# Kernel optimization log

Measured on AMD Instinct MI355X. Metric: run time of the kernel, lower is better.

The kernel has to match this reference:

```python
import jax, jax.numpy as jnp
import numpy as np
from jax.ops import segment_sum

N_NODES = 50000
N_EDGES = 800000
IN_CH, HIDDEN, OUT_CH = 64, 128, 64


def _glorot(key, fan_in, fan_out):
    lim = np.sqrt(6.0 / (fan_in + fan_out)).astype(np.float32)
    return jax.random.uniform(key, (fan_in, fan_out), jnp.float32, -lim, lim)


def setup_inputs() -> dict:
    key = jax.random.key(0)
    ks = jax.random.split(key, 10)
    x = jax.random.normal(ks[0], (N_NODES, IN_CH), jnp.float32)
    edge_index = jax.random.randint(ks[1], (2, N_EDGES), 0, N_NODES, jnp.int64)
    return {
        "x": x,
        "edge_index": edge_index,
        # GINConv1 MLP: Linear(in,hidden) -> ReLU -> Linear(hidden,hidden)
        "W1": _glorot(ks[2], IN_CH, HIDDEN),
        "b1": jnp.zeros((HIDDEN,), jnp.float32),
        "W2": _glorot(ks[3], HIDDEN, HIDDEN),
        "b2": jnp.zeros((HIDDEN,), jnp.float32),
        "eps1": jnp.zeros((), jnp.float32),
        # GINConv2 MLP: Linear(hidden,hidden) -> ReLU -> Linear(hidden,out)
        "W3": _glorot(ks[4], HIDDEN, HIDDEN),
        "b3": jnp.zeros((HIDDEN,), jnp.float32),
        "W4": _glorot(ks[5], HIDDEN, OUT_CH),
        "b4": jnp.zeros((OUT_CH,), jnp.float32),
        "eps2": jnp.zeros((), jnp.float32),
    }


def _gin_conv(x, src, dst, eps, Wa, ba, Wb, bb):
    # message = x[src]; aggregate = scatter-add at dst (sum aggregation)
    agg = segment_sum(x[src], dst, num_segments=N_NODES)  # [N, C]
    h = (1.0 + eps) * x + agg
    h = jax.nn.relu(h @ Wa + ba)
    return h @ Wb + bb


def reference(x, edge_index, W1, b1, W2, b2, eps1, W3, b3, W4, b4, eps2):
    src, dst = edge_index[0], edge_index[1]
    h1 = jax.nn.relu(_gin_conv(x, src, dst, eps1, W1, b1, W2, b2))
    h2 = _gin_conv(h1, src, dst, eps2, W3, b3, W4, b4)
    return h2
```

## Files before the change

kernel.cpp:

```cpp
#include <hip/hip_runtime.h>

#define N_NODES 50000
#define N_EDGES 800000
#define IN_CH 64
#define HIDDEN 128
#define OUT_CH 64
#define CAP 64

typedef unsigned short ushort_t;
typedef unsigned int uint_t;
typedef __attribute__((ext_vector_type(8))) short short8;
typedef __attribute__((ext_vector_type(4))) float f32x4;

__device__ __forceinline__ float bits2f(unsigned int u16) {
    union { unsigned int i; float f; } v;
    v.i = (u16 & 0xFFFFu) << 16;
    return v.f;
}

__device__ __forceinline__ ushort_t f2bits(float f) {
    union { float f; unsigned int i; } v;
    v.f = f;
    unsigned int x = v.i;
    if ((x & 0x7F800000u) == 0x7F800000u) return (ushort_t)(x >> 16);
    unsigned int r = (x + 0x7FFFu + ((x >> 16) & 1u)) >> 16;
    return (ushort_t)r;
}

__device__ __forceinline__ uint_t pack2(float x, float y) {
    return (uint_t)f2bits(x) | ((uint_t)f2bits(y) << 16);
}

__global__ __launch_bounds__(256) void append_k(const int* __restrict__ ei,
                                                int* __restrict__ cnt,
                                                ushort_t* __restrict__ bucket) {
    int e = blockIdx.x * 256 + threadIdx.x;
    if (e >= N_EDGES) return;
    int src = ei[e];
    int dst = ei[N_EDGES + e];
    int pos = atomicAdd(&cnt[dst], 1);
    if (pos < CAP) bucket[(size_t)dst * CAP + pos] = (ushort_t)src;
}

__global__ __launch_bounds__(256) void cvt_k(const float* __restrict__ x,
                                             uint_t* __restrict__ xu) {
    int i = blockIdx.x * 256 + threadIdx.x;
    if (i >= N_NODES * IN_CH / 2) return;
    float2 v = ((const float2*)x)[i];
    xu[i] = pack2(v.x, v.y);
}

__global__ __launch_bounds__(256) void pack_k(const float* __restrict__ W,
                                              ushort_t* __restrict__ out,
                                              int K, int C) {
    int tid = blockIdx.x * 256 + threadIdx.x;
    if (tid >= K * C) return;
    int j = tid & 7;
    int l = (tid >> 3) & 63;
    int rest = tid >> 9;
    int KC = K >> 5;
    int kc = rest % KC;
    int nt = rest / KC;
    int k = kc * 32 + (l >> 4) * 8 + j;
    int n = nt * 16 + (l & 15);
    out[tid] = f2bits(W[(size_t)k * C + n]);
}

__global__ __launch_bounds__(256) void gather1(const uint_t* __restrict__ xu,
                                               const int* __restrict__ cnt,
                                               const ushort_t* __restrict__ bucket,
                                               const float* __restrict__ eps1,
                                               uint_t* __restrict__ agg1b) {
    int tid = threadIdx.x;
    int li = tid & 31;
    int n = blockIdx.x * 8 + (tid >> 5);
    uint_t v = xu[(size_t)n * 32 + li];
    float se = 1.0f + eps1[0];
    float a0 = se * bits2f(v), a1 = se * bits2f(v >> 16);
    float b0 = 0.f, b1 = 0.f, c0 = 0.f, c1 = 0.f, d0 = 0.f, d1 = 0.f;
    int cn = cnt[n]; if (cn > CAP) cn = CAP;
    const ushort_t* bk = bucket + (size_t)n * CAP;
    int i = 0;
    for (; i + 3 < cn; i += 4) {
        ushort4 e4 = *(const ushort4*)(bk + i);
        uint_t u0 = xu[(size_t)e4.x * 32 + li];
        uint_t u1 = xu[(size_t)e4.y * 32 + li];
        uint_t u2 = xu[(size_t)e4.z * 32 + li];
        uint_t u3 = xu[(size_t)e4.w * 32 + li];
        a0 += bits2f(u0); a1 += bits2f(u0 >> 16);
        b0 += bits2f(u1); b1 += bits2f(u1 >> 16);
        c0 += bits2f(u2); c1 += bits2f(u2 >> 16);
        d0 += bits2f(u3); d1 += bits2f(u3 >> 16);
    }
    for (; i < cn; i++) {
        uint_t u = xu[(size_t)bk[i] * 32 + li];
        a0 += bits2f(u); a1 += bits2f(u >> 16);
    }
    agg1b[(size_t)n * 32 + li] = pack2(a0 + b0 + c0 + d0, a1 + b1 + c1 + d1);
}

__global__ __launch_bounds__(256) void gather2(const ushort_t* __restrict__ h1,
                                               const int* __restrict__ cnt,
                                               const ushort_t* __restrict__ bucket,
                                               const float* __restrict__ eps2,
                                               uint_t* __restrict__ agg2b) {
    int lane = threadIdx.x & 63;
    int n = blockIdx.x * 4 + (threadIdx.x >> 6);
    const uint_t* h1u = (const uint_t*)h1;
    uint_t v = h1u[(size_t)n * 64 + lane];
    float se = 1.0f + eps2[0];
    float a0 = se * bits2f(v), a1 = se * bits2f(v >> 16);
    float b0 = 0.f, b1 = 0.f, c0 = 0.f, c1 = 0.f, d0 = 0.f, d1 = 0.f;
    int cn = cnt[n]; if (cn > CAP) cn = CAP;
    const ushort_t* bk = bucket + (size_t)n * CAP;
    int i = 0;
    for (; i + 3 < cn; i += 4) {
        ushort4 e4 = *(const ushort4*)(bk + i);
        uint_t u0 = h1u[(size_t)e4.x * 64 + lane];
        uint_t u1 = h1u[(size_t)e4.y * 64 + lane];
        uint_t u2 = h1u[(size_t)e4.z * 64 + lane];
        uint_t u3 = h1u[(size_t)e4.w * 64 + lane];
        a0 += bits2f(u0); a1 += bits2f(u0 >> 16);
        b0 += bits2f(u1); b1 += bits2f(u1 >> 16);
        c0 += bits2f(u2); c1 += bits2f(u2 >> 16);
        d0 += bits2f(u3); d1 += bits2f(u3 >> 16);
    }
    for (; i < cn; i++) {
        uint_t u = h1u[(size_t)bk[i] * 64 + lane];
        a0 += bits2f(u); a1 += bits2f(u >> 16);
    }
    agg2b[(size_t)n * 64 + lane] = pack2(a0 + b0 + c0 + d0, a1 + b1 + c1 + d1);
}

#define TPAD 136

__global__ __launch_bounds__(256) void mlp1(const ushort_t* __restrict__ agg1b,
                                            const ushort_t* __restrict__ pW1,
                                            const float* __restrict__ b1,
                                            const ushort_t* __restrict__ pW2,
                                            const float* __restrict__ b2,
                                            ushort_t* __restrict__ h1) {
    __shared__ __align__(16) ushort_t t[64][TPAD];
    int w = threadIdx.x >> 6;
    int l = threadIdx.x & 63;
    int q = l >> 4;
    int c = l & 15;
    int m0 = blockIdx.x * 64 + w * 16;
    int node = m0 + c;
    int nc = node < N_NODES ? node : 0;
    short8 a0 = *(const short8*)(agg1b + (size_t)nc * IN_CH + q * 8);
    short8 a1 = *(const short8*)(agg1b + (size_t)nc * IN_CH + 32 + q * 8);
#pragma unroll
    for (int nt = 0; nt < 8; nt++) {
        float bb = b1[nt * 16 + c];
        f32x4 acc = {bb, bb, bb, bb};
        short8 bf0 = *(const short8*)(pW1 + (size_t)((nt * 2 + 0) * 64 + l) * 8);
        short8 bf1 = *(const short8*)(pW1 + (size_t)((nt * 2 + 1) * 64 + l) * 8);
        acc = __builtin_amdgcn_mfma_f32_16x16x32_bf16(a0, bf0, acc, 0, 0, 0);
        acc = __builtin_amdgcn_mfma_f32_16x16x32_bf16(a1, bf1, acc, 0, 0, 0);
#pragma unroll
        for (int r = 0; r < 4; r++)
            t[w * 16 + q * 4 + r][nt * 16 + c] = f2bits(fmaxf(acc[r], 0.0f));
    }
    __syncthreads();
    short8 A[4];
#pragma unroll
    for (int kc = 0; kc < 4; kc++)
        A[kc] = *(const short8*)&t[w * 16 + c][kc * 32 + q * 8];
#pragma unroll
    for (int nt = 0; nt < 8; nt++) {
        float bb = b2[nt * 16 + c];
        f32x4 acc = {bb, bb, bb, bb};
#pragma unroll
        for (int kc = 0; kc < 4; kc++) {
            short8 bf = *(const short8*)(pW2 + (size_t)((nt * 4 + kc) * 64 + l) * 8);
            acc = __builtin_amdgcn_mfma_f32_16x16x32_bf16(A[kc], bf, acc, 0, 0, 0);
        }
#pragma unroll
        for (int r = 0; r < 4; r++) {
            int rr = m0 + q * 4 + r;
            if (rr < N_NODES)
                h1[(size_t)rr * HIDDEN + nt * 16 + c] = f2bits(fmaxf(acc[r], 0.0f));
        }
    }
}

__global__ __launch_bounds__(256) void mlp2(const ushort_t* __restrict__ agg2b,
                                            const ushort_t* __restrict__ pW3,
                                            const float* __restrict__ b3,
                                            const ushort_t* __restrict__ pW4,
                                            const float* __restrict__ b4,
                                            float* __restrict__ out) {
    __shared__ __align__(16) ushort_t t[64][TPAD];
    int w = threadIdx.x >> 6;
    int l = threadIdx.x & 63;
    int q = l >> 4;
    int c = l & 15;
    int m0 = blockIdx.x * 64 + w * 16;
    int node = m0 + c;
    int nc = node < N_NODES ? node : 0;
    short8 A[4];
#pragma unroll
    for (int kc = 0; kc < 4; kc++)
        A[kc] = *(const short8*)(agg2b + (size_t)nc * HIDDEN + kc * 32 + q * 8);
#pragma unroll
    for (int nt = 0; nt < 8; nt++) {
        float bb = b3[nt * 16 + c];
        f32x4 acc = {bb, bb, bb, bb};
#pragma unroll
        for (int kc = 0; kc < 4; kc++) {
            short8 bf = *(const short8*)(pW3 + (size_t)((nt * 4 + kc) * 64 + l) * 8);
            acc = __builtin_amdgcn_mfma_f32_16x16x32_bf16(A[kc], bf, acc, 0, 0, 0);
        }
#pragma unroll
        for (int r = 0; r < 4; r++)
            t[w * 16 + q * 4 + r][nt * 16 + c] = f2bits(fmaxf(acc[r], 0.0f));
    }
    __syncthreads();
    short8 B[4];
#pragma unroll
    for (int kc = 0; kc < 4; kc++)
        B[kc] = *(const short8*)&t[w * 16 + c][kc * 32 + q * 8];
#pragma unroll
    for (int nt = 0; nt < 4; nt++) {
        float bb = b4[nt * 16 + c];
        f32x4 acc = {bb, bb, bb, bb};
#pragma unroll
        for (int kc = 0; kc < 4; kc++) {
            short8 bf = *(const short8*)(pW4 + (size_t)((nt * 4 + kc) * 64 + l) * 8);
            acc = __builtin_amdgcn_mfma_f32_16x16x32_bf16(B[kc], bf, acc, 0, 0, 0);
        }
#pragma unroll
        for (int r = 0; r < 4; r++) {
            int rr = m0 + q * 4 + r;
            if (rr < N_NODES)
                out[(size_t)rr * OUT_CH + nt * 16 + c] = acc[r];
        }
    }
}

extern "C" void kernel_launch(void* const* d_in, const int* in_sizes, int n_in,
                              void* d_out, int out_size, void* d_ws, size_t ws_size,
                              hipStream_t stream) {
    const float* x    = (const float*)d_in[0];
    const int*   ei   = (const int*)d_in[1];
    const float* W1   = (const float*)d_in[2];
    const float* b1   = (const float*)d_in[3];
    const float* W2   = (const float*)d_in[4];
    const float* b2   = (const float*)d_in[5];
    const float* eps1 = (const float*)d_in[6];
    const float* W3   = (const float*)d_in[7];
    const float* b3   = (const float*)d_in[8];
    const float* W4   = (const float*)d_in[9];
    const float* b4   = (const float*)d_in[10];
    const float* eps2 = (const float*)d_in[11];
    float* out = (float*)d_out;

    ushort_t* wsU = (ushort_t*)d_ws;
    ushort_t* agg2b = wsU;
    uint_t*   xb    = (uint_t*)wsU;
    ushort_t* h1    = wsU + (size_t)6400000;
    ushort_t* agg1b = wsU + (size_t)12800000;
    ushort_t* pW    = wsU + (size_t)16000000;
    ushort_t* pW1 = pW;
    ushort_t* pW2 = pW + 8192;
    ushort_t* pW3 = pW + 24576;
    ushort_t* pW4 = pW + 40960;
    int* cnt        = (int*)(wsU + (size_t)16049152);
    ushort_t* bucket = (ushort_t*)(cnt + N_NODES);

    hipMemsetAsync(cnt, 0, N_NODES * sizeof(int), stream);
    append_k<<<(N_EDGES + 255) / 256, 256, 0, stream>>>(ei, cnt, bucket);

    pack_k<<<(IN_CH * HIDDEN + 255) / 256, 256, 0, stream>>>(W1, pW1, IN_CH, HIDDEN);
    pack_k<<<(HIDDEN * HIDDEN + 255) / 256, 256, 0, stream>>>(W2, pW2, HIDDEN, HIDDEN);
    pack_k<<<(HIDDEN * HIDDEN + 255) / 256, 256, 0, stream>>>(W3, pW3, HIDDEN, HIDDEN);
    pack_k<<<(HIDDEN * OUT_CH + 255) / 256, 256, 0, stream>>>(W4, pW4, HIDDEN, OUT_CH);

    cvt_k<<<(N_NODES * IN_CH / 2 + 255) / 256, 256, 0, stream>>>(x, xb);
    gather1<<<N_NODES / 8, 256, 0, stream>>>(xb, cnt, bucket, eps1, (uint_t*)agg1b);
    mlp1<<<(N_NODES + 63) / 64, 256, 0, stream>>>(agg1b, pW1, b1, pW2, b2, h1);

    gather2<<<N_NODES / 4, 256, 0, stream>>>(h1, cnt, bucket, eps2, (uint_t*)agg2b);
    mlp2<<<(N_NODES + 63) / 64, 256, 0, stream>>>(agg2b, pW3, b3, pW4, b4, out);
}
```

Before: 229.0 us.

## Build CSR buckets via two-pass LDS binning and fuse prep kernels

Replaces the global-atomic edge append with a two-stage binning scheme. First, blocks bin edges by destination range into shared memory and flush them to per-bin segments. Second, one block per 256-node bin builds the bucket list in LDS and writes it out with coalesced vector stores. The memset, weight-pack kernels and x conversion are merged into fewer launches. The goal is to cut scattered global atomics and launch overhead. The cost is an extra pass over the edges and a fixed per-bin segment capacity that could overflow.

After: 198.0 us. 1.16x faster.

```diff
diff --git a/kernel.cpp b/kernel.cpp
--- a/kernel.cpp
+++ b/kernel.cpp
@@ -6,6 +6,10 @@
 #define HIDDEN 128
 #define OUT_CH 64
 #define CAP 64
+#define BINS 196
+#define CHUNK 3125
+#define LCAP 48
+#define SEGCAP 4608
 
 typedef unsigned short ushort_t;
 typedef unsigned int uint_t;
@@ -31,39 +35,103 @@
     return (uint_t)f2bits(x) | ((uint_t)f2bits(y) << 16);
 }
 
-__global__ __launch_bounds__(256) void append_k(const int* __restrict__ ei,
-                                                int* __restrict__ cnt,
-                                                ushort_t* __restrict__ bucket) {
-    int e = blockIdx.x * 256 + threadIdx.x;
-    if (e >= N_EDGES) return;
-    int src = ei[e];
-    int dst = ei[N_EDGES + e];
-    int pos = atomicAdd(&cnt[dst], 1);
-    if (pos < CAP) bucket[(size_t)dst * CAP + pos] = (ushort_t)src;
-}
-
-__global__ __launch_bounds__(256) void cvt_k(const float* __restrict__ x,
-                                             uint_t* __restrict__ xu) {
-    int i = blockIdx.x * 256 + threadIdx.x;
-    if (i >= N_NODES * IN_CH / 2) return;
-    float2 v = ((const float2*)x)[i];
-    xu[i] = pack2(v.x, v.y);
-}
-
-__global__ __launch_bounds__(256) void pack_k(const float* __restrict__ W,
-                                              ushort_t* __restrict__ out,
-                                              int K, int C) {
-    int tid = blockIdx.x * 256 + threadIdx.x;
-    if (tid >= K * C) return;
-    int j = tid & 7;
-    int l = (tid >> 3) & 63;
-    int rest = tid >> 9;
-    int KC = K >> 5;
-    int kc = rest % KC;
-    int nt = rest / KC;
-    int k = kc * 32 + (l >> 4) * 8 + j;
-    int n = nt * 16 + (l & 15);
-    out[tid] = f2bits(W[(size_t)k * C + n]);
+__global__ __launch_bounds__(256) void binA(const int* __restrict__ ei,
+                                            int* __restrict__ gcur,
+                                            uint_t* __restrict__ seg) {
+    __shared__ uint_t lbin[BINS][LCAP];
+    __shared__ int lcnt[BINS];
+    __shared__ int lbase[BINS];
+    int t = threadIdx.x;
+    for (int i = t; i < BINS; i += 256) lcnt[i] = 0;
+    __syncthreads();
+    int e0 = blockIdx.x * CHUNK;
+    int e1 = e0 + CHUNK; if (e1 > N_EDGES) e1 = N_EDGES;
+    for (int e = e0 + t; e < e1; e += 256) {
+        int src = ei[e];
+        int dst = ei[N_EDGES + e];
+        int bin = dst >> 8;
+        uint_t rec = ((uint_t)src << 16) | (uint_t)(dst & 255);
+        int pos = atomicAdd(&lcnt[bin], 1);
+        if (pos < LCAP) {
+            lbin[bin][pos] = rec;
+        } else {
+            int gp = atomicAdd(&gcur[bin], 1);
+            if (gp < SEGCAP) seg[(size_t)bin * SEGCAP + gp] = rec;
+        }
+    }
+    __syncthreads();
+    for (int i = t; i < BINS; i += 256) {
+        int c = lcnt[i]; if (c > LCAP) c = LCAP;
+        lbase[i] = atomicAdd(&gcur[i], c);
+    }
+    __syncthreads();
+    int wv = t >> 6, ln = t & 63;
+    for (int i = wv; i < BINS; i += 4) {
+        int c = lcnt[i]; if (c > LCAP) c = LCAP;
+        int base = lbase[i];
+        for (int j = ln; j < c; j += 64)
+            seg[(size_t)i * SEGCAP + base + j] = lbin[i][j];
+    }
+}
+
+__global__ __launch_bounds__(256) void binB(const uint_t* __restrict__ seg,
+                                            const int* __restrict__ gcur,
+                                            int* __restrict__ cnt,
+                                            ushort_t* __restrict__ bucket) {
+    __shared__ ushort_t lb[256 * CAP];
+    __shared__ int lc[256];
+    int b = blockIdx.x;
+    int t = threadIdx.x;
+    lc[t] = 0;
+    __syncthreads();
+    int c = gcur[b]; if (c > SEGCAP) c = SEGCAP;
+    const uint_t* s = seg + (size_t)b * SEGCAP;
+    for (int i = t; i < c; i += 256) {
+        uint_t rec = s[i];
+        int ldst = rec & 255;
+        int pos = atomicAdd(&lc[ldst], 1);
+        if (pos < CAP) lb[ldst * CAP + pos] = (ushort_t)(rec >> 16);
+    }
+    __syncthreads();
+    int n0 = b * 256;
+    int nvalid = N_NODES - n0; if (nvalid > 256) nvalid = 256;
+    uint4* gb = (uint4*)(bucket + (size_t)n0 * CAP);
+    const uint4* lbv = (const uint4*)lb;
+    int total = nvalid * (CAP / 8);
+    for (int i = t; i < total; i += 256) gb[i] = lbv[i];
+    if (t < nvalid) cnt[n0 + t] = lc[t];
+}
+
+__global__ __launch_bounds__(256) void prep_k(const float* __restrict__ x,
+                                              uint_t* __restrict__ xu,
+                                              const float* __restrict__ W1, ushort_t* __restrict__ pW1,
+                                              const float* __restrict__ W2, ushort_t* __restrict__ pW2,
+                                              const float* __restrict__ W3, ushort_t* __restrict__ pW3,
+                                              const float* __restrict__ W4, ushort_t* __restrict__ pW4) {
+    int b = blockIdx.x;
+    if (b < 192) {
+        const float* W; ushort_t* o; int K, C, b0;
+        if (b < 32)       { W = W1; o = pW1; K = IN_CH;  C = HIDDEN; b0 = 0; }
+        else if (b < 96)  { W = W2; o = pW2; K = HIDDEN; C = HIDDEN; b0 = 32; }
+        else if (b < 160) { W = W3; o = pW3; K = HIDDEN; C = HIDDEN; b0 = 96; }
+        else              { W = W4; o = pW4; K = HIDDEN; C = OUT_CH; b0 = 160; }
+        int tid = (b - b0) * 256 + threadIdx.x;
+        int j = tid & 7;
+        int l = (tid >> 3) & 63;
+        int rest = tid >> 9;
+        int KC = K >> 5;
+        int kc = rest % KC;
+        int nt = rest / KC;
+        int k = kc * 32 + (l >> 4) * 8 + j;
+        int n = nt * 16 + (l & 15);
+        o[tid] = f2bits(W[(size_t)k * C + n]);
+    } else {
+        int i = (b - 192) * 256 + threadIdx.x;
+        if (i < N_NODES * IN_CH / 2) {
+            float2 v = ((const float2*)x)[i];
+            xu[i] = pack2(v.x, v.y);
+        }
+    }
 }
 
 __global__ __launch_bounds__(256) void gather1(const uint_t* __restrict__ xu,
@@ -266,18 +334,18 @@
     ushort_t* pW2 = pW + 8192;
     ushort_t* pW3 = pW + 24576;
     ushort_t* pW4 = pW + 40960;
-    int* cnt        = (int*)(wsU + (size_t)16049152);
+    int* cnt         = (int*)(wsU + (size_t)16049152);
     ushort_t* bucket = (ushort_t*)(cnt + N_NODES);
-
-    hipMemsetAsync(cnt, 0, N_NODES * sizeof(int), stream);
-    append_k<<<(N_EDGES + 255) / 256, 256, 0, stream>>>(ei, cnt, bucket);
-
-    pack_k<<<(IN_CH * HIDDEN + 255) / 256, 256, 0, stream>>>(W1, pW1, IN_CH, HIDDEN);
-    pack_k<<<(HIDDEN * HIDDEN + 255) / 256, 256, 0, stream>>>(W2, pW2, HIDDEN, HIDDEN);
-    pack_k<<<(HIDDEN * HIDDEN + 255) / 256, 256, 0, stream>>>(W3, pW3, HIDDEN, HIDDEN);
-    pack_k<<<(HIDDEN * OUT_CH + 255) / 256, 256, 0, stream>>>(W4, pW4, HIDDEN, OUT_CH);
-
-    cvt_k<<<(N_NODES * IN_CH / 2 + 255) / 256, 256, 0, stream>>>(x, xb);
+    int* gcur        = (int*)(bucket + (size_t)N_NODES * CAP);
+    uint_t* seg      = (uint_t*)(gcur + 256);
+
+    hipMemsetAsync(gcur, 0, BINS * sizeof(int), stream);
+    binA<<<(N_EDGES + CHUNK - 1) / CHUNK, 256, 0, stream>>>(ei, gcur, seg);
+    binB<<<BINS, 256, 0, stream>>>(seg, gcur, cnt, bucket);
+
+    prep_k<<<192 + (N_NODES * IN_CH / 2 + 255) / 256, 256, 0, stream>>>(
+        x, xb, W1, pW1, W2, pW2, W3, pW3, W4, pW4);
+
     gather1<<<N_NODES / 8, 256, 0, stream>>>(xb, cnt, bucket, eps1, (uint_t*)agg1b);
     mlp1<<<(N_NODES + 63) / 64, 256, 0, stream>>>(agg1b, pW1, b1, pW2, b2, h1);
 
```
